# Optimization experiments

Measured on AMD Instinct MI355X. Metric: run time of the kernel, lower is better.

Reference implementation:

```python
import jax, jax.numpy as jnp
import numpy as np

B, S, D, H = 2, 2048, 1024, 16  # batch, seq, rep_dim, num_heads
DH = D // H
MASK_VALUE = -1e-06  # value passed by MHAttention to masked_softmax (NOT -1e6)


def setup_inputs() -> dict:
    key = jax.random.key(0)
    ks = jax.random.split(key, 16)
    def xavier(k, shape):
        fan_in, fan_out = shape[0], shape[1]
        limit = float(np.sqrt(6.0 / (fan_in + fan_out)))
        return jax.random.uniform(k, shape, jnp.float32, -limit, limit)
    return {
        "queries": jax.random.normal(ks[0], (B, S, D), jnp.float32),
        "keys": jax.random.normal(ks[1], (B, S, D), jnp.float32),
        "values": jax.random.normal(ks[2], (B, S, D), jnp.float32),
        "thresholds": jax.random.randint(ks[3], (B,), 1, S + 1, jnp.int32),
        # Linear params stored as (in, out) so y = x @ W + b
        "Wq": xavier(ks[4], (D, D)), "bq": jnp.zeros((D,), jnp.float32),
        "Wk": xavier(ks[5], (D, D)), "bk": jnp.zeros((D,), jnp.float32),
        "Wv": xavier(ks[6], (D, D)), "bv": jnp.zeros((D,), jnp.float32),
        "W": xavier(ks[7], (DH, DH)),  # learnable bilinear attention matrix
        "Wo": xavier(ks[8], (D, D)), "bo": jnp.zeros((D,), jnp.float32),
    }


def reference(queries, keys, values, thresholds, Wq, bq, Wk, bk, Wv, bv, W, Wo, bo):
    def split_heads(x):  # (B,S,D) -> (B,H,S,DH)
        return x.reshape(B, S, H, DH).transpose(0, 2, 1, 3)

    Q = split_heads(queries @ Wq + bq)
    K = split_heads(keys @ Wk + bk)
    V = split_heads(values @ Wv + bv)

    # bilinear scores: (Q @ W) @ K^T, no 1/sqrt(d) scaling in original
    scores = jnp.einsum("bhqd,bhkd->bhqk", Q @ W, K)
    # mask key positions >= threshold[b] with MASK_VALUE before softmax
    keep = jnp.arange(S)[None, None, None, :] < thresholds[:, None, None, None]
    scores = jnp.where(keep, scores, MASK_VALUE)
    attn = jax.nn.softmax(scores, axis=-1)

    out = jnp.einsum("bhqk,bhkd->bhqd", attn, V)
    out = out.transpose(0, 2, 1, 3).reshape(B, S, D)  # merge heads
    return out @ Wo + bo
```

## Files before the change

### kernel.cpp

```cpp
#include <hip/hip_runtime.h>
#include <hip/hip_bf16.h>

#define D_MODEL 1024
#define NHEADS  16
#define DH      64
#define SEQ     2048
#define BATCH   2

#define LOG2E 1.4426950408889634f
#define MASKB2 (-1e-6f * LOG2E)
#define DEFER_THR 11.5456f
#define NEG_INF (-__builtin_inff())

typedef __attribute__((ext_vector_type(8))) short short8;
typedef __attribute__((ext_vector_type(4))) short short4v;
typedef __attribute__((ext_vector_type(4))) float f32x4;

#define AS1C(p) ((const __attribute__((address_space(1))) void*)(p))
#define AS3(p)  ((__attribute__((address_space(3))) void*)(p))

union PB { short4v s4; unsigned int u[2]; };

static __device__ __forceinline__ float fexp2(float x) {
    return __builtin_amdgcn_exp2f(x);
}

static __device__ __forceinline__ unsigned int pk2(float lo, float hi) {
    __hip_bfloat16 a = __float2bfloat16(lo), b = __float2bfloat16(hi);
    unsigned short au = *(unsigned short*)&a, bu = *(unsigned short*)&b;
    return (unsigned int)au | ((unsigned int)bu << 16);
}

__global__ __launch_bounds__(256) void fold_q_kernel(const float* __restrict__ Wq,
                                                     const float* __restrict__ bq,
                                                     const float* __restrict__ W,
                                                     __hip_bfloat16* __restrict__ WqT,
                                                     float* __restrict__ bq2) {
    const int t = threadIdx.x;
    const int c0 = blockIdx.x * 32;
    const int h = c0 >> 6, j0 = c0 & 63;

    if (blockIdx.y == 32) {
        if (t < 32) {
            int col = c0 + t, j = col & 63;
            float s = 0.f;
#pragma unroll
            for (int d = 0; d < DH; ++d) s += bq[h * DH + d] * W[d * DH + j];
            bq2[col] = s * LOG2E;
        }
        return;
    }

    const int r0 = blockIdx.y * 32;
    __shared__ float sWq[32][68];
    __shared__ float sW[64][36];
    __shared__ float sOut[32][33];

    {
        int lr = t >> 3, lc8 = (t & 7) * 8;
        const float* src = Wq + (size_t)(r0 + lr) * D_MODEL + h * DH + lc8;
        *(float4*)&sWq[lr][lc8]     = *(const float4*)(src);
        *(float4*)&sWq[lr][lc8 + 4] = *(const float4*)(src + 4);
        int d = t >> 2, c8 = (t & 3) * 8;
        const float* wsrc = W + (size_t)d * DH + j0 + c8;
        *(float4*)&sW[d][c8]     = *(const float4*)(wsrc);
        *(float4*)&sW[d][c8 + 4] = *(const float4*)(wsrc + 4);
    }
    __syncthreads();

    {
        int col_loc = t & 31, rq = t >> 5;
        float acc0 = 0.f, acc1 = 0.f, acc2 = 0.f, acc3 = 0.f;
#pragma unroll
        for (int d = 0; d < 64; ++d) {
            float wv = sW[d][col_loc];
            acc0 += sWq[rq * 4 + 0][d] * wv;
            acc1 += sWq[rq * 4 + 1][d] * wv;
            acc2 += sWq[rq * 4 + 2][d] * wv;
            acc3 += sWq[rq * 4 + 3][d] * wv;
        }
        sOut[col_loc][rq * 4 + 0] = acc0 * LOG2E;
        sOut[col_loc][rq * 4 + 1] = acc1 * LOG2E;
        sOut[col_loc][rq * 4 + 2] = acc2 * LOG2E;
        sOut[col_loc][rq * 4 + 3] = acc3 * LOG2E;
    }
    __syncthreads();

    {
        int orow = t >> 3, oc4 = (t & 7) * 4;
        __hip_bfloat16 o4[4];
#pragma unroll
        for (int i = 0; i < 4; ++i) o4[i] = __float2bfloat16(sOut[orow][oc4 + i]);
        *(short4*)(WqT + (size_t)(c0 + orow) * D_MODEL + r0 + oc4) = *(short4*)o4;
    }
}

__global__ __launch_bounds__(256) void prep_kernel(const float* __restrict__ Wk,
                                                   const float* __restrict__ Wv,
                                                   const float* __restrict__ Wo,
                                                   __hip_bfloat16* __restrict__ WkT,
                                                   __hip_bfloat16* __restrict__ WvT,
                                                   __hip_bfloat16* __restrict__ WoT,
                                                   const float* __restrict__ q,
                                                   const float* __restrict__ k,
                                                   const float* __restrict__ v,
                                                   __hip_bfloat16* __restrict__ oq,
                                                   __hip_bfloat16* __restrict__ ok,
                                                   __hip_bfloat16* __restrict__ ov) {
    __shared__ float sT[32][33];
    int blk = blockIdx.x;
    if (blk < 3072) {
        int z = blk >> 10, r = blk & 1023;
        const float* Win = (z == 0) ? Wk : (z == 1) ? Wv : Wo;
        __hip_bfloat16* Wt = (z == 0) ? WkT : (z == 1) ? WvT : WoT;
        int n0 = (r & 31) * 32, k0 = (r >> 5) * 32;
        int tx = threadIdx.x & 31, ty = threadIdx.x >> 5;
#pragma unroll
        for (int i = 0; i < 4; ++i)
            sT[ty + i * 8][tx] = Win[(size_t)(k0 + ty + i * 8) * D_MODEL + n0 + tx];
        __syncthreads();
#pragma unroll
        for (int i = 0; i < 4; ++i)
            Wt[(size_t)(n0 + ty + i * 8) * D_MODEL + k0 + tx] =
                __float2bfloat16(sT[tx][ty + i * 8]);
    } else {
        int idx = blk - 3072;
        int z = idx >> 11;
        int i = (idx & 2047) * 256 + threadIdx.x;
        const float* in = (z == 0) ? q : (z == 1) ? k : v;
        __hip_bfloat16* out = (z == 0) ? oq : (z == 1) ? ok : ov;
        float4 a = *(const float4*)(in + (size_t)i * 8);
        float4 b = *(const float4*)(in + (size_t)i * 8 + 4);
        __hip_bfloat16 o[8];
        o[0] = __float2bfloat16(a.x); o[1] = __float2bfloat16(a.y);
        o[2] = __float2bfloat16(a.z); o[3] = __float2bfloat16(a.w);
        o[4] = __float2bfloat16(b.x); o[5] = __float2bfloat16(b.y);
        o[6] = __float2bfloat16(b.z); o[7] = __float2bfloat16(b.w);
        *(short8*)(out + (size_t)i * 8) = *(short8*)o;
    }
}

#define GEMM_CORE(A_, BT_)                                                                  \
    __shared__ __hip_bfloat16 sA[2][128 * 32];                                              \
    __shared__ __hip_bfloat16 sB[2][128 * 32];                                              \
    const int t = threadIdx.x;                                                              \
    const int lane = t & 63, w = t >> 6;                                                    \
    const int g = lane >> 4, li = lane & 15;                                                \
    const int r0 = blockIdx.y * 128, c0 = blockIdx.x * 128;                                 \
    const int wr = (w >> 1) * 64, wc = (w & 1) * 64;                                        \
    f32x4 acc[4][4] = {};                                                                   \
    auto stage = [&](int bb, int k0) {                                                      \
        _Pragma("unroll")                                                                   \
        for (int i = 0; i < 2; ++i) {                                                       \
            int o = (i * 4 + w) * 1024 + lane * 16;                                         \
            int row = o >> 6, ce = (o & 63) >> 1;                                           \
            __builtin_amdgcn_global_load_lds(AS1C(A_ + (size_t)(r0 + row) * 1024 + k0 + ce),\
                                             AS3((char*)sA[bb] + (i * 4 + w) * 1024), 16, 0, 0); \
            __builtin_amdgcn_global_load_lds(AS1C(BT_ + (size_t)(c0 + row) * 1024 + k0 + ce),\
                                             AS3((char*)sB[bb] + (i * 4 + w) * 1024), 16, 0, 0); \
        }                                                                                   \
    };                                                                                      \
    stage(0, 0);                                                                            \
    asm volatile("s_waitcnt vmcnt(0)" ::: "memory");                                        \
    __syncthreads();                                                                        \
    int cur = 0;                                                                            \
    for (int k0 = 0; k0 < 1024; k0 += 32) {                                                 \
        if (k0 + 32 < 1024) stage(cur ^ 1, k0 + 32);                                        \
        short8 af[4], bf[4];                                                                \
        _Pragma("unroll")                                                                   \
        for (int m = 0; m < 4; ++m)                                                         \
            af[m] = *(const short8*)(sA[cur] + (wr + m * 16 + li) * 32 + g * 8);            \
        _Pragma("unroll")                                                                   \
        for (int n = 0; n < 4; ++n)                                                         \
            bf[n] = *(const short8*)(sB[cur] + (wc + n * 16 + li) * 32 + g * 8);            \
        _Pragma("unroll")                                                                   \
        for (int m = 0; m < 4; ++m)                                                         \
            _Pragma("unroll")                                                               \
            for (int n = 0; n < 4; ++n)                                                     \
                acc[m][n] = __builtin_amdgcn_mfma_f32_16x16x32_bf16(af[m], bf[n], acc[m][n], 0, 0, 0); \
        asm volatile("s_waitcnt vmcnt(0)" ::: "memory");                                    \
        __syncthreads();                                                                    \
        cur ^= 1;                                                                           \
    }

__global__ __launch_bounds__(256) void gemm_qkv_kernel(
    const __hip_bfloat16* __restrict__ Xq, const __hip_bfloat16* __restrict__ Xk,
    const __hip_bfloat16* __restrict__ Xv,
    const __hip_bfloat16* __restrict__ WqT, const __hip_bfloat16* __restrict__ WkT,
    const __hip_bfloat16* __restrict__ WvT,
    const float* __restrict__ bq2, const float* __restrict__ bk, const float* __restrict__ bv,
    __hip_bfloat16* __restrict__ Qp, __hip_bfloat16* __restrict__ Kp,
    __hip_bfloat16* __restrict__ Vt) {
    const int z = blockIdx.z;
    const __hip_bfloat16* A  = (z == 0) ? Xq  : (z == 1) ? Xk  : Xv;
    const __hip_bfloat16* BT = (z == 0) ? WqT : (z == 1) ? WkT : WvT;
    const float* bias        = (z == 0) ? bq2 : (z == 1) ? bk  : bv;
    __hip_bfloat16* C        = (z == 0) ? Qp  : (z == 1) ? Kp  : Vt;

    GEMM_CORE(A, BT)

#pragma unroll
    for (int m = 0; m < 4; ++m) {
#pragma unroll
        for (int n = 0; n < 4; ++n) {
            int col = c0 + wc + n * 16 + li;
            float bs = bias[col];
            int row0 = r0 + wr + m * 16 + g * 4;
            int h = col >> 6, d = col & 63;
            if (z == 2) {
                int b = row0 >> 11, s0 = row0 & 2047;
                __hip_bfloat16 o4[4];
#pragma unroll
                for (int r = 0; r < 4; ++r) o4[r] = __float2bfloat16(acc[m][n][r] + bs);
                *(short4*)(C + (((size_t)(b * NHEADS + h)) * DH + d) * SEQ + s0) = *(short4*)o4;
            } else {
#pragma unroll
                for (int r = 0; r < 4; ++r) {
                    int row = row0 + r;
                    int b = row >> 11, s = row & 2047;
                    C[(((size_t)(b * NHEADS + h)) * SEQ + s) * DH + d] =
                        __float2bfloat16(acc[m][n][r] + bs);
                }
            }
        }
    }
}

__global__ __launch_bounds__(256) void gemm_out_kernel(
    const __hip_bfloat16* __restrict__ A, const __hip_bfloat16* __restrict__ BT,
    const float* __restrict__ bias, float* __restrict__ C) {
    GEMM_CORE(A, BT)
#pragma unroll
    for (int m = 0; m < 4; ++m) {
#pragma unroll
        for (int n = 0; n < 4; ++n) {
            int col = c0 + wc + n * 16 + li;
            float bs = bias[col];
            int row0 = r0 + wr + m * 16 + g * 4;
#pragma unroll
            for (int r = 0; r < 4; ++r)
                C[(size_t)(row0 + r) * D_MODEL + col] = acc[m][n][r] + bs;
        }
    }
}

__global__ __launch_bounds__(256) void vsum_kernel(const __hip_bfloat16* __restrict__ Vt,
                                                   const int* __restrict__ thresholds,
                                                   float* __restrict__ Vsum) {
    int bh = blockIdx.x, b = bh >> 4;
    int thresh = thresholds[b];
    int loop_end = min(SEQ, ((thresh + 63) >> 6) << 6);
    int t = threadIdx.x;
    int dh = t >> 2, sub = t & 3;
    const __hip_bfloat16* row = Vt + ((size_t)bh * DH + dh) * SEQ;
    float s = 0.f;
    for (int s0 = loop_end + sub * 8; s0 < SEQ; s0 += 32) {
        short8 v = *(const short8*)(row + s0);
#pragma unroll
        for (int j = 0; j < 8; ++j) {
            unsigned short us = (unsigned short)v[j];
            s += __bfloat162float(*(__hip_bfloat16*)&us);
        }
    }
    s += __shfl_xor(s, 1);
    s += __shfl_xor(s, 2);
    if (sub == 0) Vsum[bh * DH + dh] = s;
}

__global__ __launch_bounds__(256) void attn_mfma_kernel(
    const __hip_bfloat16* __restrict__ Qp,
    const __hip_bfloat16* __restrict__ Kp,
    const __hip_bfloat16* __restrict__ Vt,
    const int* __restrict__ thresholds,
    const float* __restrict__ Vsum,
    __hip_bfloat16* __restrict__ AO) {
    __shared__ char lds[32768];
    char* sK  = lds;
    char* sVT = lds + 16384;

    const int t = threadIdx.x, lane = t & 63, w = t >> 6;
    const int g = lane >> 4, li = lane & 15;
    const int bh_i = blockIdx.y;
    const int bh = ((bh_i & 1) << 4) | (bh_i >> 1);
    const int b = bh >> 4, h = bh & 15;
    const int q0 = blockIdx.x * 64;
    const int thresh = thresholds[b];
    const int loop_end = min(SEQ, ((thresh + 63) >> 6) << 6);
    const __hip_bfloat16* Qb = Qp + (size_t)bh * SEQ * DH;
    const __hip_bfloat16* Kb = Kp + (size_t)bh * SEQ * DH;
    const __hip_bfloat16* Vb = Vt + (size_t)bh * DH * SEQ;

    short8 qf[2];
#pragma unroll
    for (int kb = 0; kb < 2; ++kb)
        qf[kb] = *(const short8*)(Qb + (size_t)(q0 + w * 16 + li) * DH + kb * 32 + g * 8);

    f32x4 Oacc[4] = {};
    float mrun = NEG_INF, lrun = 0.f;

    auto stageK = [&](int bb, int kv) {
#pragma unroll
        for (int i = 0; i < 2; ++i) {
            int o = i * 4096 + w * 1024 + lane * 16;
            int key = o >> 7, slot = (o & 127) >> 4;
            __builtin_amdgcn_global_load_lds(
                AS1C(Kb + (size_t)(kv + key) * DH + ((slot ^ (key & 7)) << 3)),
                AS3(sK + bb * 8192 + i * 4096 + w * 1024), 16, 0, 0);
        }
    };
    auto stageV = [&](int bb, int kv) {
#pragma unroll
        for (int i = 0; i < 2; ++i) {
            int o = i * 4096 + w * 1024 + lane * 16;
            int dh = o >> 7, slot = (o & 127) >> 4;
            __builtin_amdgcn_global_load_lds(
                AS1C(Vb + (size_t)dh * SEQ + kv + ((slot ^ (dh & 7)) << 3)),
                AS3(sVT + bb * 8192 + i * 4096 + w * 1024), 16, 0, 0);
        }
    };

    stageK(0, 0); stageV(0, 0);
    asm volatile("s_waitcnt vmcnt(0)" ::: "memory");
    __syncthreads();

    int cur = 0;
    for (int kv0 = 0; kv0 < loop_end; kv0 += 64) {
        int nxt = kv0 + 64;
        if (nxt < loop_end) { stageK(cur ^ 1, nxt); stageV(cur ^ 1, nxt); }

        f32x4 S[4] = {};
        __builtin_amdgcn_s_setprio(1);
#pragma unroll
        for (int kb = 0; kb < 2; ++kb) {
            short8 kf[4];
#pragma unroll
            for (int n = 0; n < 4; ++n) {
                int key = 16 * n + li;
                kf[n] = *(const short8*)(sK + cur * 8192 + key * 128 +
                                         (((4 * kb + g) ^ (key & 7)) << 4));
            }
#pragma unroll
            for (int n = 0; n < 4; ++n)
                S[n] = __builtin_amdgcn_mfma_f32_16x16x32_bf16(kf[n], qf[kb], S[n], 0, 0, 0);
        }
        __builtin_amdgcn_s_setprio(0);

        if (kv0 + 64 > thresh) {
            int tr = thresh - kv0 - 4 * g;
#pragma unroll
            for (int n = 0; n < 4; ++n)
#pragma unroll
                for (int rr = 0; rr < 4; ++rr)
                    if (16 * n + rr >= tr) S[n][rr] = MASKB2;
        }

        float mx = S[0][0];
#pragma unroll
        for (int n = 0; n < 4; ++n)
#pragma unroll
            for (int rr = 0; rr < 4; ++rr) mx = fmaxf(mx, S[n][rr]);
        mx = fmaxf(mx, __shfl_xor(mx, 16));
        mx = fmaxf(mx, __shfl_xor(mx, 32));
        float pmax = mx;

        if (__any(pmax > mrun + DEFER_THR)) {
            float mn = fmaxf(mrun, pmax);
            float alpha = fexp2(mrun - mn);
            lrun *= alpha;
#pragma unroll
            for (int n = 0; n < 4; ++n)
#pragma unroll
                for (int rr = 0; rr < 4; ++rr) Oacc[n][rr] *= alpha;
            mrun = mn;
        }

        short4v pb[4];
        float rs = 0.f;
#pragma unroll
        for (int n = 0; n < 4; ++n) {
#pragma unroll
            for (int rr = 0; rr < 4; ++rr) {
                float p = fexp2(S[n][rr] - mrun);
                S[n][rr] = p;
                rs += p;
            }
            PB u;
            u.u[0] = pk2(S[n][0], S[n][1]);
            u.u[1] = pk2(S[n][2], S[n][3]);
            pb[n] = u.s4;
        }
        rs += __shfl_xor(rs, 16);
        rs += __shfl_xor(rs, 32);
        lrun += rs;

        __builtin_amdgcn_s_setprio(1);
#pragma unroll
        for (int ks = 0; ks < 4; ++ks) {
            int slot = 2 * ks + (g >> 1);
            int sub8 = 8 * (g & 1);
#pragma unroll
            for (int n = 0; n < 4; ++n) {
                int dh = 16 * n + li;
                short4v va = *(const short4v*)(sVT + cur * 8192 + dh * 128 +
                                               ((slot ^ (dh & 7)) << 4) + sub8);
                Oacc[n] = __builtin_amdgcn_mfma_f32_16x16x16bf16_1k(va, pb[ks], Oacc[n], 0, 0, 0);
            }
        }
        __builtin_amdgcn_s_setprio(0);

        asm volatile("s_waitcnt vmcnt(0)" ::: "memory");
        __syncthreads();
        cur ^= 1;
    }

    int nmask = SEQ - loop_end;
    if (nmask > 0) {
        const float* vs = Vsum + bh * DH;
        f32x4 vsf[4];
#pragma unroll
        for (int n = 0; n < 4; ++n) vsf[n] = *(const f32x4*)(vs + 16 * n + 4 * g);
        float pu = fexp2(MASKB2 - mrun);
        lrun += (float)nmask * pu;
#pragma unroll
        for (int n = 0; n < 4; ++n)
#pragma unroll
            for (int rr = 0; rr < 4; ++rr) Oacc[n][rr] += pu * vsf[n][rr];
    }

    float linv = 1.0f / lrun;
    int q = q0 + w * 16 + li;
#pragma unroll
    for (int n = 0; n < 4; ++n) {
        __hip_bfloat16 o4[4];
#pragma unroll
        for (int rr = 0; rr < 4; ++rr) o4[rr] = __float2bfloat16(Oacc[n][rr] * linv);
        *(short4*)(AO + (size_t)(b * SEQ + q) * D_MODEL + h * DH + 16 * n + 4 * g) =
            *(short4*)o4;
    }
}

extern "C" void kernel_launch(void* const* d_in, const int* in_sizes, int n_in,
                              void* d_out, int out_size, void* d_ws, size_t ws_size,
                              hipStream_t stream) {
    const float* queries    = (const float*)d_in[0];
    const float* keys       = (const float*)d_in[1];
    const float* values     = (const float*)d_in[2];
    const int*   thresholds = (const int*)d_in[3];
    const float* Wq = (const float*)d_in[4];
    const float* bq = (const float*)d_in[5];
    const float* Wk = (const float*)d_in[6];
    const float* bk = (const float*)d_in[7];
    const float* Wv = (const float*)d_in[8];
    const float* bv = (const float*)d_in[9];
    const float* W  = (const float*)d_in[10];
    const float* Wo = (const float*)d_in[11];
    const float* bo = (const float*)d_in[12];
    float* out = (float*)d_out;

    char* wsb = (char*)d_ws;
    float* bq2  = (float*)wsb;
    float* Vsum = (float*)(wsb + 4096);
    __hip_bfloat16* XqB = (__hip_bfloat16*)(wsb + 16384);
    __hip_bfloat16* XkB = XqB + (1 << 22);
    __hip_bfloat16* XvB = XkB + (1 << 22);
    __hip_bfloat16* WqT = XvB + (1 << 22);
    __hip_bfloat16* WkT = WqT + (1 << 20);
    __hip_bfloat16* WvT = WkT + (1 << 20);
    __hip_bfloat16* WoT = WvT + (1 << 20);
    __hip_bfloat16* QpB = WoT + (1 << 20);
    __hip_bfloat16* KpB = QpB + (1 << 22);
    __hip_bfloat16* VtB = KpB + (1 << 22);
    __hip_bfloat16* AOB = XqB;

    fold_q_kernel<<<dim3(32, 33), 256, 0, stream>>>(Wq, bq, W, WqT, bq2);
    prep_kernel<<<9216, 256, 0, stream>>>(Wk, Wv, Wo, WkT, WvT, WoT,
                                          queries, keys, values, XqB, XkB, XvB);

    gemm_qkv_kernel<<<dim3(8, 32, 3), 256, 0, stream>>>(XqB, XkB, XvB, WqT, WkT, WvT,
                                                        bq2, bk, bv, QpB, KpB, VtB);
    vsum_kernel<<<32, 256, 0, stream>>>(VtB, thresholds, Vsum);

    attn_mfma_kernel<<<dim3(32, 32), 256, 0, stream>>>(QpB, KpB, VtB, thresholds, Vsum, AOB);

    gemm_out_kernel<<<dim3(8, 32), 256, 0, stream>>>(AOB, WoT, bo, out);
}
```

Before: 161.3 us.

## Merge prep kernels, swizzle GEMM tiles, shrink attention blocks, defer row-sum reduction

The Q-fold and the transpose/convert prep kernels become one launch, which removes a kernel launch and lets the two halves overlap. The GEMM block index is remapped so that consecutive blocks walk down columns, aiming at better L2 reuse of weight tiles. The attention kernel moves to 128-thread blocks of 32 queries with a 32x64 grid to increase block count and occupancy, and the K/V staging loops are adjusted to match. The per-iteration softmax row-sum shuffles are replaced by one reduction after the loop. Smaller blocks reload K/V tiles more often per query.

```diff
diff --git a/kernel.cpp b/kernel.cpp
--- a/kernel.cpp
+++ b/kernel.cpp
@@ -31,90 +31,79 @@
     return (unsigned int)au | ((unsigned int)bu << 16);
 }
 
-__global__ __launch_bounds__(256) void fold_q_kernel(const float* __restrict__ Wq,
-                                                     const float* __restrict__ bq,
-                                                     const float* __restrict__ W,
-                                                     __hip_bfloat16* __restrict__ WqT,
-                                                     float* __restrict__ bq2) {
+__global__ __launch_bounds__(256) void prep_all_kernel(
+    const float* __restrict__ Wq, const float* __restrict__ bq, const float* __restrict__ W,
+    __hip_bfloat16* __restrict__ WqT, float* __restrict__ bq2,
+    const float* __restrict__ Wk, const float* __restrict__ Wv, const float* __restrict__ Wo,
+    __hip_bfloat16* __restrict__ WkT, __hip_bfloat16* __restrict__ WvT,
+    __hip_bfloat16* __restrict__ WoT,
+    const float* __restrict__ q, const float* __restrict__ k, const float* __restrict__ v,
+    __hip_bfloat16* __restrict__ oq, __hip_bfloat16* __restrict__ ok,
+    __hip_bfloat16* __restrict__ ov) {
+    const int blk = blockIdx.x;
     const int t = threadIdx.x;
-    const int c0 = blockIdx.x * 32;
-    const int h = c0 >> 6, j0 = c0 & 63;
-
-    if (blockIdx.y == 32) {
-        if (t < 32) {
-            int col = c0 + t, j = col & 63;
-            float s = 0.f;
-#pragma unroll
-            for (int d = 0; d < DH; ++d) s += bq[h * DH + d] * W[d * DH + j];
-            bq2[col] = s * LOG2E;
-        }
-        return;
-    }
-
-    const int r0 = blockIdx.y * 32;
-    __shared__ float sWq[32][68];
-    __shared__ float sW[64][36];
-    __shared__ float sOut[32][33];
-
-    {
-        int lr = t >> 3, lc8 = (t & 7) * 8;
-        const float* src = Wq + (size_t)(r0 + lr) * D_MODEL + h * DH + lc8;
-        *(float4*)&sWq[lr][lc8]     = *(const float4*)(src);
-        *(float4*)&sWq[lr][lc8 + 4] = *(const float4*)(src + 4);
-        int d = t >> 2, c8 = (t & 3) * 8;
-        const float* wsrc = W + (size_t)d * DH + j0 + c8;
-        *(float4*)&sW[d][c8]     = *(const float4*)(wsrc);
-        *(float4*)&sW[d][c8 + 4] = *(const float4*)(wsrc + 4);
-    }
-    __syncthreads();
-
-    {
-        int col_loc = t & 31, rq = t >> 5;
-        float acc0 = 0.f, acc1 = 0.f, acc2 = 0.f, acc3 = 0.f;
-#pragma unroll
-        for (int d = 0; d < 64; ++d) {
-            float wv = sW[d][col_loc];
-            acc0 += sWq[rq * 4 + 0][d] * wv;
-            acc1 += sWq[rq * 4 + 1][d] * wv;
-            acc2 += sWq[rq * 4 + 2][d] * wv;
-            acc3 += sWq[rq * 4 + 3][d] * wv;
-        }
-        sOut[col_loc][rq * 4 + 0] = acc0 * LOG2E;
-        sOut[col_loc][rq * 4 + 1] = acc1 * LOG2E;
-        sOut[col_loc][rq * 4 + 2] = acc2 * LOG2E;
-        sOut[col_loc][rq * 4 + 3] = acc3 * LOG2E;
-    }
-    __syncthreads();
-
-    {
-        int orow = t >> 3, oc4 = (t & 7) * 4;
-        __hip_bfloat16 o4[4];
-#pragma unroll
-        for (int i = 0; i < 4; ++i) o4[i] = __float2bfloat16(sOut[orow][oc4 + i]);
-        *(short4*)(WqT + (size_t)(c0 + orow) * D_MODEL + r0 + oc4) = *(short4*)o4;
-    }
-}
-
-__global__ __launch_bounds__(256) void prep_kernel(const float* __restrict__ Wk,
-                                                   const float* __restrict__ Wv,
-                                                   const float* __restrict__ Wo,
-                                                   __hip_bfloat16* __restrict__ WkT,
-                                                   __hip_bfloat16* __restrict__ WvT,
-                                                   __hip_bfloat16* __restrict__ WoT,
-                                                   const float* __restrict__ q,
-                                                   const float* __restrict__ k,
-                                                   const float* __restrict__ v,
-                                                   __hip_bfloat16* __restrict__ oq,
-                                                   __hip_bfloat16* __restrict__ ok,
-                                                   __hip_bfloat16* __restrict__ ov) {
-    __shared__ float sT[32][33];
-    int blk = blockIdx.x;
-    if (blk < 3072) {
-        int z = blk >> 10, r = blk & 1023;
+
+    if (blk < 1056) {
+        const int c0 = (blk & 31) * 32;
+        const int yy = blk >> 5;
+        const int h = c0 >> 6, j0 = c0 & 63;
+        if (yy == 32) {
+            if (t < 32) {
+                int col = c0 + t, j = col & 63;
+                float s = 0.f;
+#pragma unroll
+                for (int d = 0; d < DH; ++d) s += bq[h * DH + d] * W[d * DH + j];
+                bq2[col] = s * LOG2E;
+            }
+            return;
+        }
+        const int r0 = yy * 32;
+        __shared__ float sWq[32][68];
+        __shared__ float sW[64][36];
+        __shared__ float sOut[32][33];
+        {
+            int lr = t >> 3, lc8 = (t & 7) * 8;
+            const float* src = Wq + (size_t)(r0 + lr) * D_MODEL + h * DH + lc8;
+            *(float4*)&sWq[lr][lc8]     = *(const float4*)(src);
+            *(float4*)&sWq[lr][lc8 + 4] = *(const float4*)(src + 4);
+            int d = t >> 2, c8 = (t & 3) * 8;
+            const float* wsrc = W + (size_t)d * DH + j0 + c8;
+            *(float4*)&sW[d][c8]     = *(const float4*)(wsrc);
+            *(float4*)&sW[d][c8 + 4] = *(const float4*)(wsrc + 4);
+        }
+        __syncthreads();
+        {
+            int col_loc = t & 31, rq = t >> 5;
+            float acc0 = 0.f, acc1 = 0.f, acc2 = 0.f, acc3 = 0.f;
+#pragma unroll
+            for (int d = 0; d < 64; ++d) {
+                float wv = sW[d][col_loc];
+                acc0 += sWq[rq * 4 + 0][d] * wv;
+                acc1 += sWq[rq * 4 + 1][d] * wv;
+                acc2 += sWq[rq * 4 + 2][d] * wv;
+                acc3 += sWq[rq * 4 + 3][d] * wv;
+            }
+            sOut[col_loc][rq * 4 + 0] = acc0 * LOG2E;
+            sOut[col_loc][rq * 4 + 1] = acc1 * LOG2E;
+            sOut[col_loc][rq * 4 + 2] = acc2 * LOG2E;
+            sOut[col_loc][rq * 4 + 3] = acc3 * LOG2E;
+        }
+        __syncthreads();
+        {
+            int orow = t >> 3, oc4 = (t & 7) * 4;
+            __hip_bfloat16 o4[4];
+#pragma unroll
+            for (int i = 0; i < 4; ++i) o4[i] = __float2bfloat16(sOut[orow][oc4 + i]);
+            *(short4*)(WqT + (size_t)(c0 + orow) * D_MODEL + r0 + oc4) = *(short4*)o4;
+        }
+    } else if (blk < 4128) {
+        __shared__ float sT[32][33];
+        int r = blk - 1056;
+        int z = r >> 10; r &= 1023;
         const float* Win = (z == 0) ? Wk : (z == 1) ? Wv : Wo;
         __hip_bfloat16* Wt = (z == 0) ? WkT : (z == 1) ? WvT : WoT;
         int n0 = (r & 31) * 32, k0 = (r >> 5) * 32;
-        int tx = threadIdx.x & 31, ty = threadIdx.x >> 5;
+        int tx = t & 31, ty = t >> 5;
 #pragma unroll
         for (int i = 0; i < 4; ++i)
             sT[ty + i * 8][tx] = Win[(size_t)(k0 + ty + i * 8) * D_MODEL + n0 + tx];
@@ -124,9 +113,9 @@
             Wt[(size_t)(n0 + ty + i * 8) * D_MODEL + k0 + tx] =
                 __float2bfloat16(sT[tx][ty + i * 8]);
     } else {
-        int idx = blk - 3072;
+        int idx = blk - 4128;
         int z = idx >> 11;
-        int i = (idx & 2047) * 256 + threadIdx.x;
+        int i = (idx & 2047) * 256 + t;
         const float* in = (z == 0) ? q : (z == 1) ? k : v;
         __hip_bfloat16* out = (z == 0) ? oq : (z == 1) ? ok : ov;
         float4 a = *(const float4*)(in + (size_t)i * 8);
@@ -146,7 +135,9 @@
     const int t = threadIdx.x;                                                              \
     const int lane = t & 63, w = t >> 6;                                                    \
     const int g = lane >> 4, li = lane & 15;                                                \
-    const int r0 = blockIdx.y * 128, c0 = blockIdx.x * 128;                                 \
+    const int lin = blockIdx.y * 8 + blockIdx.x;                                            \
+    const int ob = (lin & 7) * 32 + (lin >> 3);                                             \
+    const int r0 = (ob >> 3) * 128, c0 = (ob & 7) * 128;                                    \
     const int wr = (w >> 1) * 64, wc = (w & 1) * 64;                                        \
     f32x4 acc[4][4] = {};                                                                   \
     auto stage = [&](int bb, int k0) {                                                      \
@@ -267,7 +258,7 @@
     if (sub == 0) Vsum[bh * DH + dh] = s;
 }
 
-__global__ __launch_bounds__(256) void attn_mfma_kernel(
+__global__ __launch_bounds__(128) void attn_mfma_kernel(
     const __hip_bfloat16* __restrict__ Qp,
     const __hip_bfloat16* __restrict__ Kp,
     const __hip_bfloat16* __restrict__ Vt,
@@ -280,10 +271,8 @@
 
     const int t = threadIdx.x, lane = t & 63, w = t >> 6;
     const int g = lane >> 4, li = lane & 15;
-    const int bh_i = blockIdx.y;
-    const int bh = ((bh_i & 1) << 4) | (bh_i >> 1);
-    const int b = bh >> 4, h = bh & 15;
-    const int q0 = blockIdx.x * 64;
+    const int bh = blockIdx.x, b = bh >> 4, h = bh & 15;
+    const int q0 = blockIdx.y * 32;
     const int thresh = thresholds[b];
     const int loop_end = min(SEQ, ((thresh + 63) >> 6) << 6);
     const __hip_bfloat16* Qb = Qp + (size_t)bh * SEQ * DH;
@@ -296,26 +285,26 @@
         qf[kb] = *(const short8*)(Qb + (size_t)(q0 + w * 16 + li) * DH + kb * 32 + g * 8);
 
     f32x4 Oacc[4] = {};
-    float mrun = NEG_INF, lrun = 0.f;
+    float mrun = NEG_INF, lpart = 0.f;
 
     auto stageK = [&](int bb, int kv) {
 #pragma unroll
-        for (int i = 0; i < 2; ++i) {
-            int o = i * 4096 + w * 1024 + lane * 16;
+        for (int i = 0; i < 4; ++i) {
+            int o = i * 2048 + w * 1024 + lane * 16;
             int key = o >> 7, slot = (o & 127) >> 4;
             __builtin_amdgcn_global_load_lds(
                 AS1C(Kb + (size_t)(kv + key) * DH + ((slot ^ (key & 7)) << 3)),
-                AS3(sK + bb * 8192 + i * 4096 + w * 1024), 16, 0, 0);
+                AS3(sK + bb * 8192 + i * 2048 + w * 1024), 16, 0, 0);
         }
     };
     auto stageV = [&](int bb, int kv) {
 #pragma unroll
-        for (int i = 0; i < 2; ++i) {
-            int o = i * 4096 + w * 1024 + lane * 16;
+        for (int i = 0; i < 4; ++i) {
+            int o = i * 2048 + w * 1024 + lane * 16;
             int dh = o >> 7, slot = (o & 127) >> 4;
             __builtin_amdgcn_global_load_lds(
                 AS1C(Vb + (size_t)dh * SEQ + kv + ((slot ^ (dh & 7)) << 3)),
-                AS3(sVT + bb * 8192 + i * 4096 + w * 1024), 16, 0, 0);
+                AS3(sVT + bb * 8192 + i * 2048 + w * 1024), 16, 0, 0);
         }
     };
 
@@ -366,7 +355,7 @@
         if (__any(pmax > mrun + DEFER_THR)) {
             float mn = fmaxf(mrun, pmax);
             float alpha = fexp2(mrun - mn);
-            lrun *= alpha;
+            lpart *= alpha;
 #pragma unroll
             for (int n = 0; n < 4; ++n)
 #pragma unroll
@@ -375,23 +364,19 @@
         }
 
         short4v pb[4];
-        float rs = 0.f;
 #pragma unroll
         for (int n = 0; n < 4; ++n) {
 #pragma unroll
             for (int rr = 0; rr < 4; ++rr) {
                 float p = fexp2(S[n][rr] - mrun);
                 S[n][rr] = p;
-                rs += p;
+                lpart += p;
             }
             PB u;
             u.u[0] = pk2(S[n][0], S[n][1]);
             u.u[1] = pk2(S[n][2], S[n][3]);
             pb[n] = u.s4;
         }
-        rs += __shfl_xor(rs, 16);
-        rs += __shfl_xor(rs, 32);
-        lrun += rs;
 
         __builtin_amdgcn_s_setprio(1);
 #pragma unroll
@@ -412,6 +397,10 @@
         __syncthreads();
         cur ^= 1;
     }
+
+    float lrun = lpart;
+    lrun += __shfl_xor(lrun, 16);
+    lrun += __shfl_xor(lrun, 32);
 
     int nmask = SEQ - loop_end;
     if (nmask > 0) {
@@ -472,15 +461,15 @@
     __hip_bfloat16* VtB = KpB + (1 << 22);
     __hip_bfloat16* AOB = XqB;
 
-    fold_q_kernel<<<dim3(32, 33), 256, 0, stream>>>(Wq, bq, W, WqT, bq2);
-    prep_kernel<<<9216, 256, 0, stream>>>(Wk, Wv, Wo, WkT, WvT, WoT,
-                                          queries, keys, values, XqB, XkB, XvB);
+    prep_all_kernel<<<10272, 256, 0, stream>>>(Wq, bq, W, WqT, bq2,
+                                               Wk, Wv, Wo, WkT, WvT, WoT,
+                                               queries, keys, values, XqB, XkB, XvB);
 
     gemm_qkv_kernel<<<dim3(8, 32, 3), 256, 0, stream>>>(XqB, XkB, XvB, WqT, WkT, WvT,
                                                         bq2, bk, bv, QpB, KpB, VtB);
     vsum_kernel<<<32, 256, 0, stream>>>(VtB, thresholds, Vsum);
 
-    attn_mfma_kernel<<<dim3(32, 32), 256, 0, stream>>>(QpB, KpB, VtB, thresholds, Vsum, AOB);
+    attn_mfma_kernel<<<dim3(32, 64), 128, 0, stream>>>(QpB, KpB, VtB, thresholds, Vsum, AOB);
 
     gemm_out_kernel<<<dim3(8, 32), 256, 0, stream>>>(AOB, WoT, bo, out);
 }
```

After: 177.7 us. 1.1x slower.
